# Kernel optimization log

Hardware: AMD Instinct MI355X
Metric: run time of the kernel (lower is better)

Reference implementation:

```python
import jax, jax.numpy as jnp
import numpy as np

N, E, IN, HID, EE, L, NB = 20000, 256000, 64, 128, 32, 3, 8


def _silu(x):
    return x * jax.nn.sigmoid(x)


def setup_inputs() -> dict:
    key = jax.random.key(0)
    ks = list(jax.random.split(key, 32))

    def nrm(k, shape, fan_in):
        return jax.random.normal(k, shape, dtype=jnp.float32) / np.sqrt(fan_in)

    inp = {}
    inp["H_t"] = jax.random.normal(ks[0], (N, IN), dtype=jnp.float32)
    inp["X_t"] = jax.random.normal(ks[1], (N, 3), dtype=jnp.float32)
    inp["cond_embedding"] = jax.random.normal(ks[2], (N, HID), dtype=jnp.float32)
    inp["t"] = jax.random.uniform(ks[3], (N,), dtype=jnp.float32)
    inp["edges"] = jax.random.randint(ks[4], (2, E), 0, N)
    inp["edge_types"] = jax.random.randint(ks[5], (E,), 0, 2)
    inp["generate_mask"] = jax.random.bernoulli(ks[6], 0.7, (N,))
    inp["batch_ids"] = jnp.sort(jax.random.randint(ks[7], (N,), 0, NB))
    # input MLP: (IN + 2*HID) -> HID -> HID -> HID, 3 linear layers
    d0 = IN + 2 * HID
    inp["mlp_W0"] = nrm(ks[8], (d0, HID), d0)
    inp["mlp_b0"] = jnp.zeros((HID,), jnp.float32)
    inp["mlp_W1"] = nrm(ks[9], (HID, HID), HID)
    inp["mlp_b1"] = jnp.zeros((HID,), jnp.float32)
    inp["mlp_W2"] = nrm(ks[10], (HID, HID), HID)
    inp["mlp_b2"] = jnp.zeros((HID,), jnp.float32)
    inp["edge_table"] = jax.random.normal(ks[11], (2, EE), dtype=jnp.float32)
    # encoder (EGNN-style message passing), stacked over L layers
    de = 2 * HID + 1 + EE  # [h_src, h_dst, dist^2, edge_embed]
    inp["We"] = nrm(ks[12], (L, de, HID), de)
    inp["be"] = jnp.zeros((L, HID), jnp.float32)
    inp["Wx"] = nrm(ks[13], (L, HID, 1), HID)
    inp["bx"] = jnp.zeros((L, 1), jnp.float32)
    inp["Wh"] = nrm(ks[14], (L, 2 * HID, HID), 2 * HID)
    inp["bh"] = jnp.zeros((L, HID), jnp.float32)
    inp["h2i_W"] = nrm(ks[15], (HID, IN), HID)
    inp["h2i_b"] = jnp.zeros((IN,), jnp.float32)
    return inp


def reference(H_t, X_t, cond_embedding, t, mlp_W0, mlp_b0, mlp_W1, mlp_b1,
              mlp_W2, mlp_b2, edge_table, We, be, Wx, bx, Wh, bh,
              h2i_W, h2i_b, edges, edge_types, generate_mask, batch_ids):
    n = H_t.shape[0]
    hid = mlp_W2.shape[1]
    # sinusoidal time embedding (dim = hidden_size)
    half = hid // 2
    freqs = jnp.exp(jnp.arange(half, dtype=jnp.float32) * (-np.log(10000.0) / (half - 1)))
    ang = t[:, None] * freqs[None, :]
    t_embed = jnp.concatenate([jnp.sin(ang), jnp.cos(ang)], axis=-1)  # (N, hid)
    # input MLP
    feat = jnp.concatenate([H_t, cond_embedding, t_embed], axis=-1)
    h = jax.nn.relu(feat @ mlp_W0 + mlp_b0)
    h = jax.nn.relu(h @ mlp_W1 + mlp_b1)
    h = h @ mlp_W2 + mlp_b2
    eemb = edge_table[edge_types]  # (E, EE)
    src, dst = edges[0], edges[1]
    cnt = jax.ops.segment_sum(jnp.ones((src.shape[0], 1), h.dtype), dst, num_segments=n)
    x = X_t
    for l in range(We.shape[0]):
        diff = x[src] - x[dst]                              # (E, 3)
        d2 = jnp.sum(diff * diff, axis=-1, keepdims=True)   # (E, 1)
        m_in = jnp.concatenate([h[src], h[dst], d2, eemb], axis=-1)
        msg = _silu(m_in @ We[l] + be[l])                   # (E, hid)
        w = msg @ Wx[l] + bx[l]                             # (E, 1)
        agg_x = jax.ops.segment_sum(diff * w, dst, num_segments=n)
        x = x + agg_x / (cnt + 1.0)
        agg_m = jax.ops.segment_sum(msg, dst, num_segments=n)
        h = h + _silu(jnp.concatenate([h, agg_m], axis=-1) @ Wh[l] + bh[l])
    mask = generate_mask[:, None]
    v_X = jnp.where(mask, x, jnp.zeros_like(x))
    v_H = jnp.where(mask, h @ h2i_W + h2i_b, 0.0)
    return (v_H, v_X)
```

## Files before the change

kernel.cpp:

```cpp
#include <hip/hip_runtime.h>
#include <math.h>

#define NN 20000
#define NE 256000
#define IN_DIM 64
#define HID 128
#define DE 289
#define D0 320
#define TILE_E 64
#define NB64 313
#define NUB 8
#define SRCMASK 0x3FFFFFFF

typedef unsigned short u16;
typedef unsigned int u32;
typedef unsigned long long u64;
typedef __attribute__((ext_vector_type(8))) short short8;
typedef __attribute__((ext_vector_type(4))) float float4v;

#define OFF_WE   0
#define OFF_W0   122880
#define OFF_W1   163840
#define OFF_W2   180224
#define OFF_WH   196608
#define OFF_H2I  294912
#define PACK_TOT 303104
#define PREP_TOT (PACK_TOT + 1152 + NN)

static __device__ __forceinline__ u16 f2bf(float f) {
    unsigned int u = __float_as_uint(f);
    u += 0x7fffu + ((u >> 16) & 1u);
    return (u16)(u >> 16);
}
static __device__ __forceinline__ float bf2f(u16 s) {
    return __uint_as_float(((unsigned int)s) << 16);
}
static __device__ __forceinline__ float bflo(u32 u) { return bf2f((u16)(u & 0xffffu)); }
static __device__ __forceinline__ float bfhi(u32 u) { return bf2f((u16)(u >> 16)); }
static __device__ __forceinline__ u32 pack2(float a, float b) {
    return (u32)f2bf(a) | ((u32)f2bf(b) << 16);
}
static __device__ __forceinline__ uint4 pack8(const float* v) {
    uint4 r;
    r.x = (u32)f2bf(v[0]) | ((u32)f2bf(v[1]) << 16);
    r.y = (u32)f2bf(v[2]) | ((u32)f2bf(v[3]) << 16);
    r.z = (u32)f2bf(v[4]) | ((u32)f2bf(v[5]) << 16);
    r.w = (u32)f2bf(v[6]) | ((u32)f2bf(v[7]) << 16);
    return r;
}
static __device__ __forceinline__ float silu(float v) {
    return v * (1.f / (1.f + __expf(-v)));
}

__global__ __launch_bounds__(256) void hist_kernel(
    const float* __restrict__ X_t, const int* __restrict__ edges,
    float* __restrict__ x, int* __restrict__ deg)
{
    int gid = blockIdx.x * blockDim.x + threadIdx.x;
    int stride = gridDim.x * blockDim.x;
    for (int i = gid; i < NN * 3; i += stride) x[i] = X_t[i];
    for (int e = gid; e < NE; e += stride)
        atomicAdd(&deg[edges[NE + e]], 1);
}

__global__ __launch_bounds__(1024) void scan_kernel(
    const int* __restrict__ deg, int* __restrict__ row_start, int* __restrict__ head)
{
    __shared__ int s[1024];
    int tx = threadIdx.x;
    const int per = (NN + 1023) / 1024;
    int st = tx * per, en = st + per;
    if (st > NN) st = NN;
    if (en > NN) en = NN;
    int sum = 0;
    for (int i = st; i < en; ++i) sum += deg[i];
    s[tx] = sum;
    __syncthreads();
    for (int off = 1; off < 1024; off <<= 1) {
        int t = (tx >= off) ? s[tx - off] : 0;
        __syncthreads();
        s[tx] += t;
        __syncthreads();
    }
    int run = (tx == 0) ? 0 : s[tx - 1];
    for (int i = st; i < en; ++i) {
        row_start[i] = run; head[i] = run; run += deg[i];
    }
    if (tx == 1023) row_start[NN] = run;
}

__global__ __launch_bounds__(256) void scatter_kernel(
    const int* __restrict__ edges, const int* __restrict__ etype,
    int* __restrict__ head,
    int* __restrict__ src_s)
{
    int gid = blockIdx.x * blockDim.x + threadIdx.x;
    int stride = gridDim.x * blockDim.x;
    for (int e = gid; e < NE; e += stride) {
        int d = edges[NE + e];
        int p = atomicAdd(&head[d], 1);
        src_s[p] = edges[e] | (etype[e] << 30);
    }
}

__global__ __launch_bounds__(256) void prep_kernel(
    const float* __restrict__ We, const float* __restrict__ W0,
    const float* __restrict__ W1, const float* __restrict__ W2,
    const float* __restrict__ Wh, const float* __restrict__ h2i,
    const float* __restrict__ edge_table, const float* __restrict__ be,
    u16* __restrict__ Bp, float* __restrict__ tv, float* __restrict__ wed2,
    int* __restrict__ deg)
{
    int idx = blockIdx.x * 256 + threadIdx.x;
    if (idx < PACK_TOT) {
        const float* src; int N = 128, Ksrc; int r;
        if (idx < OFF_W0) {
            int layer = idx / 40960; r = idx - layer * 40960;
            src = We + (size_t)layer * DE * HID; Ksrc = DE;
        } else if (idx < OFF_W1) { r = idx - OFF_W0; src = W0; Ksrc = 320; }
        else if (idx < OFF_W2)   { r = idx - OFF_W1; src = W1; Ksrc = 128; }
        else if (idx < OFF_WH)   { r = idx - OFF_W2; src = W2; Ksrc = 128; }
        else if (idx < OFF_H2I) {
            int t = idx - OFF_WH; int layer = t / 32768; r = t - layer * 32768;
            src = Wh + (size_t)layer * 256 * HID; Ksrc = 256;
        } else { r = idx - OFF_H2I; src = h2i; Ksrc = 128; N = 64; }
        int ntc = N / 16;
        int j = r & 7, lane = (r >> 3) & 63;
        int rem = r >> 9;
        int nt = rem % ntc, ks = rem / ntc;
        int k = ks * 32 + ((lane >> 4) << 3) + j;
        int c = nt * 16 + (lane & 15);
        Bp[idx] = f2bf((k < Ksrc) ? src[(size_t)k * N + c] : 0.f);
    } else if (idx < PACK_TOT + 768) {
        int q = idx - PACK_TOT;
        int f = q & 127, t = (q >> 7) & 1, l = q >> 8;
        float acc = be[l * 128 + f];
        const float* W = We + (size_t)l * DE * HID;
        #pragma unroll
        for (int k = 0; k < 32; ++k)
            acc += edge_table[t * 32 + k] * W[(size_t)(257 + k) * HID + f];
        tv[l * 256 + t * 128 + f] = acc;
    } else if (idx < PACK_TOT + 1152) {
        int r = idx - PACK_TOT - 768;
        int f = r & 127, l = r >> 7;
        wed2[l * 128 + f] = We[(size_t)l * DE * HID + (size_t)256 * HID + f];
    } else if (idx < PREP_TOT) {
        deg[idx - PACK_TOT - 1152] = 0;
    }
}

__global__ __launch_bounds__(256) void node_mlp_mfma_kernel(
    const float* __restrict__ H_t, const float* __restrict__ cond,
    const float* __restrict__ t_in,
    const u16* __restrict__ W0p, const float* __restrict__ b0,
    const u16* __restrict__ W1p, const float* __restrict__ b1,
    const u16* __restrict__ W2p, const float* __restrict__ b2,
    const u16* __restrict__ WEp,
    u16* __restrict__ Csrc, u16* __restrict__ Cdst,
    float* __restrict__ h, u16* __restrict__ h_bf)
{
    __shared__ u16 s_A[64 * 64];
    __shared__ u16 s_B[64 * 128];
    __shared__ u16 s_h[64 * 128];
    __shared__ float s_t[64];

    int tx = threadIdx.x;
    int n0 = blockIdx.x * 64;
    int l = tx & 63, w = tx >> 6;
    int mt_base = (w & 1) * 2, nt_base = (w >> 1) * 4;
    const float cfr = -logf(10000.f) / 63.f;

    if (tx < 64) s_t[tx] = (n0 + tx < NN) ? t_in[n0 + tx] : 0.f;

    float4v acc[2][4];
    #pragma unroll
    for (int mi = 0; mi < 2; ++mi)
        #pragma unroll
        for (int ni = 0; ni < 4; ++ni) acc[mi][ni] = (float4v){0.f,0.f,0.f,0.f};

    for (int t = 0; t < 5; ++t) {
        __syncthreads();
        #pragma unroll
        for (int it = 0; it < 2; ++it) {
            int flat = it * 256 + tx;
            int n = flat >> 3, sl = flat & 7;
            int c = sl ^ (n & 7);
            int k0 = t * 64 + c * 8;
            float tv8[8];
            int gn = n0 + n;
            if (gn < NN) {
                if (k0 < 192) {
                    const float* src = (k0 < 64) ? &H_t[(size_t)gn * IN_DIM + k0]
                                                 : &cond[(size_t)gn * HID + (k0 - 64)];
                    float4 a = *(const float4*)src;
                    float4 b = *(const float4*)(src + 4);
                    tv8[0]=a.x; tv8[1]=a.y; tv8[2]=a.z; tv8[3]=a.w;
                    tv8[4]=b.x; tv8[5]=b.y; tv8[6]=b.z; tv8[7]=b.w;
                } else {
                    float tvv = s_t[n];
                    int jj = (k0 - 192) & 63;
                    bool is_sin = (k0 < 256);
                    #pragma unroll
                    for (int jx = 0; jx < 8; ++jx) {
                        float ang = tvv * __expf(cfr * (float)(jj + jx));
                        tv8[jx] = is_sin ? __sinf(ang) : __cosf(ang);
                    }
                }
            } else {
                #pragma unroll
                for (int jx = 0; jx < 8; ++jx) tv8[jx] = 0.f;
            }
            *(uint4*)&s_A[n * 64 + sl * 8] = pack8(tv8);
        }
        #pragma unroll
        for (int it = 0; it < 4; ++it) {
            int flat = it * 256 + tx;
            ((uint4*)s_B)[flat] = ((const uint4*)(W0p + (size_t)t * 8192))[flat];
        }
        __syncthreads();
        #pragma unroll
        for (int s = 0; s < 2; ++s) {
            short8 af[2], bfv[4];
            #pragma unroll
            for (int mi = 0; mi < 2; ++mi) {
                int m = (mt_base + mi) * 16 + (l & 15);
                int c = s * 4 + (l >> 4);
                int slot = c ^ (l & 7);
                af[mi] = *(const short8*)(s_A + m * 64 + slot * 8);
            }
            #pragma unroll
            for (int ni = 0; ni < 4; ++ni)
                bfv[ni] = *(const short8*)(s_B + ((s * 8 + nt_base + ni) * 64 + l) * 8);
            #pragma unroll
            for (int mi = 0; mi < 2; ++mi)
                #pragma unroll
                for (int ni = 0; ni < 4; ++ni)
                    acc[mi][ni] = __builtin_amdgcn_mfma_f32_16x16x32_bf16(
                        af[mi], bfv[ni], acc[mi][ni], 0, 0, 0);
        }
    }
    #pragma unroll
    for (int mi = 0; mi < 2; ++mi) {
        #pragma unroll
        for (int ni = 0; ni < 4; ++ni) {
            int f = (nt_base + ni) * 16 + (l & 15);
            float bv = b0[f];
            #pragma unroll
            for (int r = 0; r < 4; ++r) {
                int m = (mt_base + mi) * 16 + (l >> 4) * 4 + r;
                float v = fmaxf(acc[mi][ni][r] + bv, 0.f);
                int slot = (f >> 3) ^ (m & 7);
                s_h[m * 128 + slot * 8 + (f & 7)] = f2bf(v);
            }
            acc[mi][ni] = (float4v){0.f,0.f,0.f,0.f};
        }
    }
    for (int t = 0; t < 2; ++t) {
        __syncthreads();
        #pragma unroll
        for (int it = 0; it < 4; ++it) {
            int flat = it * 256 + tx;
            ((uint4*)s_B)[flat] = ((const uint4*)(W1p + (size_t)t * 8192))[flat];
        }
        __syncthreads();
        #pragma unroll
        for (int s = 0; s < 2; ++s) {
            short8 af[2], bfv[4];
            #pragma unroll
            for (int mi = 0; mi < 2; ++mi) {
                int m = (mt_base + mi) * 16 + (l & 15);
                int c = t * 8 + s * 4 + (l >> 4);
                int slot = c ^ (l & 7);
                af[mi] = *(const short8*)(s_h + m * 128 + slot * 8);
            }
            #pragma unroll
            for (int ni = 0; ni < 4; ++ni)
                bfv[ni] = *(const short8*)(s_B + ((s * 8 + nt_base + ni) * 64 + l) * 8);
            #pragma unroll
            for (int mi = 0; mi < 2; ++mi)
                #pragma unroll
                for (int ni = 0; ni < 4; ++ni)
                    acc[mi][ni] = __builtin_amdgcn_mfma_f32_16x16x32_bf16(
                        af[mi], bfv[ni], acc[mi][ni], 0, 0, 0);
        }
    }
    __syncthreads();
    #pragma unroll
    for (int mi = 0; mi < 2; ++mi) {
        #pragma unroll
        for (int ni = 0; ni < 4; ++ni) {
            int f = (nt_base + ni) * 16 + (l & 15);
            float bv = b1[f];
            #pragma unroll
            for (int r = 0; r < 4; ++r) {
                int m = (mt_base + mi) * 16 + (l >> 4) * 4 + r;
                float v = fmaxf(acc[mi][ni][r] + bv, 0.f);
                int slot = (f >> 3) ^ (m & 7);
                s_h[m * 128 + slot * 8 + (f & 7)] = f2bf(v);
            }
            acc[mi][ni] = (float4v){0.f,0.f,0.f,0.f};
        }
    }
    for (int t = 0; t < 2; ++t) {
        __syncthreads();
        #pragma unroll
        for (int it = 0; it < 4; ++it) {
            int flat = it * 256 + tx;
            ((uint4*)s_B)[flat] = ((const uint4*)(W2p + (size_t)t * 8192))[flat];
        }
        __syncthreads();
        #pragma unroll
        for (int s = 0; s < 2; ++s) {
            short8 af[2], bfv[4];
            #pragma unroll
            for (int mi = 0; mi < 2; ++mi) {
                int m = (mt_base + mi) * 16 + (l & 15);
                int c = t * 8 + s * 4 + (l >> 4);
                int slot = c ^ (l & 7);
                af[mi] = *(const short8*)(s_h + m * 128 + slot * 8);
            }
            #pragma unroll
            for (int ni = 0; ni < 4; ++ni)
                bfv[ni] = *(const short8*)(s_B + ((s * 8 + nt_base + ni) * 64 + l) * 8);
            #pragma unroll
            for (int mi = 0; mi < 2; ++mi)
                #pragma unroll
                for (int ni = 0; ni < 4; ++ni)
                    acc[mi][ni] = __builtin_amdgcn_mfma_f32_16x16x32_bf16(
                        af[mi], bfv[ni], acc[mi][ni], 0, 0, 0);
        }
    }
    __syncthreads();
    #pragma unroll
    for (int mi = 0; mi < 2; ++mi) {
        #pragma unroll
        for (int ni = 0; ni < 4; ++ni) {
            int f = (nt_base + ni) * 16 + (l & 15);
            float bv = b2[f];
            #pragma unroll
            for (int r = 0; r < 4; ++r) {
                int m = (mt_base + mi) * 16 + (l >> 4) * 4 + r;
                int gn = n0 + m;
                float v = acc[mi][ni][r] + bv;
                int slot = (f >> 3) ^ (m & 7);
                s_h[m * 128 + slot * 8 + (f & 7)] = f2bf(v);
                if (gn < NN) {
                    h[(size_t)gn * HID + f] = v;
                    h_bf[(size_t)gn * HID + f] = f2bf(v);
                }
            }
        }
    }

    for (int sd = 0; sd < 2; ++sd) {
        #pragma unroll
        for (int mi = 0; mi < 2; ++mi)
            #pragma unroll
            for (int ni = 0; ni < 4; ++ni) acc[mi][ni] = (float4v){0.f,0.f,0.f,0.f};
        #pragma unroll
        for (int th = 0; th < 2; ++th) {
            int t = sd * 2 + th;
            __syncthreads();
            #pragma unroll
            for (int it = 0; it < 4; ++it) {
                int flat = it * 256 + tx;
                ((uint4*)s_B)[flat] = ((const uint4*)(WEp + (size_t)t * 8192))[flat];
            }
            __syncthreads();
            #pragma unroll
            for (int s = 0; s < 2; ++s) {
                short8 af[2], bfv[4];
                #pragma unroll
                for (int mi = 0; mi < 2; ++mi) {
                    int m = (mt_base + mi) * 16 + (l & 15);
                    int c = th * 8 + s * 4 + (l >> 4);
                    int slot = c ^ (l & 7);
                    af[mi] = *(const short8*)(s_h + m * 128 + slot * 8);
                }
                #pragma unroll
                for (int ni = 0; ni < 4; ++ni)
                    bfv[ni] = *(const short8*)(s_B + ((s * 8 + nt_base + ni) * 64 + l) * 8);
                #pragma unroll
                for (int mi = 0; mi < 2; ++mi)
                    #pragma unroll
                    for (int ni = 0; ni < 4; ++ni)
                        acc[mi][ni] = __builtin_amdgcn_mfma_f32_16x16x32_bf16(
                            af[mi], bfv[ni], acc[mi][ni], 0, 0, 0);
            }
        }
        u16* Cout = (sd == 0) ? Csrc : Cdst;
        #pragma unroll
        for (int mi = 0; mi < 2; ++mi) {
            #pragma unroll
            for (int ni = 0; ni < 4; ++ni) {
                int fq = (nt_base + ni) * 16 + (l & 15);
                #pragma unroll
                for (int r = 0; r < 4; ++r) {
                    int m = (mt_base + mi) * 16 + (l >> 4) * 4 + r;
                    int gn = n0 + m;
                    if (gn < NN)
                        Cout[(size_t)gn * 128 + fq] = f2bf(acc[mi][ni][r]);
                }
            }
        }
    }
}

__global__ __launch_bounds__(256) void cvec_kernel(
    const u16* __restrict__ h_bf, const u16* __restrict__ WEp,
    u16* __restrict__ Csrc, u16* __restrict__ Cdst)
{
    __shared__ u16 s_A[64 * 64];
    __shared__ u16 s_B[64 * 128];

    int tx = threadIdx.x;
    int n0 = blockIdx.x * 64;
    int l = tx & 63, w = tx >> 6;
    int mt_base = (w & 1) * 2, nt_base = (w >> 1) * 4;

    float4v acc[2][2][4];
    #pragma unroll
    for (int sd = 0; sd < 2; ++sd)
        #pragma unroll
        for (int mi = 0; mi < 2; ++mi)
            #pragma unroll
            for (int ni = 0; ni < 4; ++ni)
                acc[sd][mi][ni] = (float4v){0.f,0.f,0.f,0.f};

    for (int t = 0; t < 4; ++t) {
        __syncthreads();
        #pragma unroll
        for (int it = 0; it < 2; ++it) {
            int flat = it * 256 + tx;
            int n = flat >> 3, sl = flat & 7;
            int c = sl ^ (n & 7);
            int gn = n0 + n;
            uint4 v = make_uint4(0,0,0,0);
            if (gn < NN) v = *(const uint4*)(h_bf + (size_t)gn * 128 + (t & 1) * 64 + c * 8);
            *(uint4*)&s_A[n * 64 + sl * 8] = v;
        }
        #pragma unroll
        for (int it = 0; it < 4; ++it) {
            int flat = it * 256 + tx;
            ((uint4*)s_B)[flat] = ((const uint4*)(WEp + (size_t)t * 8192))[flat];
        }
        __syncthreads();
        int sd = t >> 1;
        #pragma unroll
        for (int s = 0; s < 2; ++s) {
            short8 af[2], bfv[4];
            #pragma unroll
            for (int mi = 0; mi < 2; ++mi) {
                int m = (mt_base + mi) * 16 + (l & 15);
                int c = s * 4 + (l >> 4);
                int slot = c ^ (l & 7);
                af[mi] = *(const short8*)(s_A + m * 64 + slot * 8);
            }
            #pragma unroll
            for (int ni = 0; ni < 4; ++ni)
                bfv[ni] = *(const short8*)(s_B + ((s * 8 + nt_base + ni) * 64 + l) * 8);
            #pragma unroll
            for (int mi = 0; mi < 2; ++mi)
                #pragma unroll
                for (int ni = 0; ni < 4; ++ni)
                    acc[sd][mi][ni] = __builtin_amdgcn_mfma_f32_16x16x32_bf16(
                        af[mi], bfv[ni], acc[sd][mi][ni], 0, 0, 0);
        }
    }
    #pragma unroll
    for (int sd = 0; sd < 2; ++sd) {
        u16* Cout = (sd == 0) ? Csrc : Cdst;
        #pragma unroll
        for (int mi = 0; mi < 2; ++mi) {
            #pragma unroll
            for (int ni = 0; ni < 4; ++ni) {
                int fq = (nt_base + ni) * 16 + (l & 15);
                #pragma unroll
                for (int r = 0; r < 4; ++r) {
                    int m = (mt_base + mi) * 16 + (l >> 4) * 4 + r;
                    int gn = n0 + m;
                    if (gn < NN)
                        Cout[(size_t)gn * 128 + fq] = f2bf(acc[sd][mi][ni][r]);
                }
            }
        }
    }
}

__global__ __launch_bounds__(512, 4) void node_fused_kernel(
    float* __restrict__ h, u16* __restrict__ h_bf,
    const float* __restrict__ x_in, float* __restrict__ x_out,
    const u16* __restrict__ Csrc, const u16* __restrict__ Cdst,
    const int* __restrict__ src_s,
    const int* __restrict__ row_start,
    const float* __restrict__ tv_l, const float* __restrict__ wed2_l,
    const float* __restrict__ Wx_l, const float* __restrict__ bx_l,
    const u16* __restrict__ Whp_l, const float* __restrict__ bh_l)
{
    __shared__ u16 s_A[16 * 256];

    int tx = threadIdx.x;
    int n0 = blockIdx.x * NUB;
    int l = tx & 63, w = tx >> 6;
    int i = w;
    int gn = n0 + i;
    int p = l & 31, q = l >> 5;

    if (tx < 256) {
        int n = tx >> 4, c = tx & 15;
        int slot = c ^ (n & 7);
        uint4 v = make_uint4(0, 0, 0, 0);
        if (n < NUB) v = *(const uint4*)(h_bf + (size_t)(n0 + n) * 128 + c * 8);
        *(uint4*)&s_A[n * 256 + slot * 8] = v;
    } else if (tx < 384) {
        int n = 8 + ((tx - 256) >> 4), c = 16 + (tx & 15);
        int slot = c ^ (n & 7);
        *(uint4*)&s_A[n * 256 + slot * 8] = make_uint4(0, 0, 0, 0);
    }

    float c0[4], d01[4], wed[4], wx[4];
    {
        uint2 cd = *(const uint2*)(Cdst + (size_t)gn * 128 + p * 4);
        float cdv0 = bflo(cd.x), cdv1 = bfhi(cd.x), cdv2 = bflo(cd.y), cdv3 = bfhi(cd.y);
        float4 t0 = *(const float4*)(tv_l + p * 4);
        float4 t1 = *(const float4*)(tv_l + 128 + p * 4);
        float4 wd = *(const float4*)(wed2_l + p * 4);
        float4 wv = *(const float4*)(Wx_l + p * 4);
        c0[0] = t0.x + cdv0; c0[1] = t0.y + cdv1; c0[2] = t0.z + cdv2; c0[3] = t0.w + cdv3;
        d01[0] = t1.x - t0.x; d01[1] = t1.y - t0.y; d01[2] = t1.z - t0.z; d01[3] = t1.w - t0.w;
        wed[0] = wd.x; wed[1] = wd.y; wed[2] = wd.z; wed[3] = wd.w;
        wx[0] = wv.x; wx[1] = wv.y; wx[2] = wv.z; wx[3] = wv.w;
    }
    float bx32 = bx_l[0] * (1.f / 32.f);

    int rs = row_start[gn], re = row_start[gn + 1];
    int d = re - rs;

    float xd0 = x_in[gn * 3 + 0], xd1 = x_in[gn * 3 + 1], xd2 = x_in[gn * 3 + 2];

    float ag[4] = {0.f, 0.f, 0.f, 0.f};
    float sx = 0.f, sy = 0.f, sz = 0.f;

    for (int e0 = 0; e0 < d; e0 += 64) {
        int nchunk = d - e0; if (nchunk > 64) nchunk = 64;
        int sp_l = (l < nchunk) ? src_s[rs + e0 + l] : 0;
        float gx_l = 0.f, gy_l = 0.f, gz_l = 0.f, d2_l = 0.f;
        if (l < nchunk) {
            int sm = sp_l & SRCMASK;
            gx_l = x_in[sm * 3 + 0] - xd0;
            gy_l = x_in[sm * 3 + 1] - xd1;
            gz_l = x_in[sm * 3 + 2] - xd2;
            d2_l = gx_l * gx_l + gy_l * gy_l + gz_l * gz_l;
        }

        auto FETCH = [&](int lj, uint2& cc, float& et) {
            int spE = __shfl(sp_l, lj);
            cc = make_uint2(0u, 0u); et = 0.f;
            if (lj < nchunk) {
                cc = *(const uint2*)(Csrc + (size_t)(spE & SRCMASK) * 128 + p * 4);
                et = (float)((u32)spE >> 30);
            }
        };
        auto PROC = [&](int lj, uint2 cc, float ee) {
            float dxe = __shfl(gx_l, lj);
            float dye = __shfl(gy_l, lj);
            float dze = __shfl(gz_l, lj);
            float d2e = __shfl(d2_l, lj);
            float av[4];
            av[0] = bflo(cc.x); av[1] = bfhi(cc.x);
            av[2] = bflo(cc.y); av[3] = bfhi(cc.y);
            float wpart = bx32;
            #pragma unroll
            for (int f = 0; f < 4; ++f) {
                float t = __fmaf_rn(d2e, wed[f], c0[f]);
                t = __fmaf_rn(ee, d01[f], t);
                float v = av[f] + t;
                float m = silu(v);
                ag[f] += m;
                wpart = __fmaf_rn(m, wx[f], wpart);
            }
            sx = __fmaf_rn(dxe, wpart, sx);
            sy = __fmaf_rn(dye, wpart, sy);
            sz = __fmaf_rn(dze, wpart, sz);
        };

        int ljA = q,      ljB = q + 2,  ljC = q + 4,  ljD = q + 6;
        int ljE = q + 8,  ljF = q + 10, ljG = q + 12, ljH = q + 14;
        int ljn = q + 16;
        uint2 ccA, ccB, ccC, ccD, ccE, ccF, ccG, ccH;
        float etA, etB, etC, etD, etE, etF, etG, etH;
        FETCH(ljA, ccA, etA); FETCH(ljB, ccB, etB);
        FETCH(ljC, ccC, etC); FETCH(ljD, ccD, etD);
        FETCH(ljE, ccE, etE); FETCH(ljF, ccF, etF);
        FETCH(ljG, ccG, etG); FETCH(ljH, ccH, etH);
        while (ljA < nchunk) {
            PROC(ljA, ccA, etA); ljA = ljn; ljn += 2; FETCH(ljA, ccA, etA);
            if (ljB >= nchunk) break;
            PROC(ljB, ccB, etB); ljB = ljn; ljn += 2; FETCH(ljB, ccB, etB);
            if (ljC >= nchunk) break;
            PROC(ljC, ccC, etC); ljC = ljn; ljn += 2; FETCH(ljC, ccC, etC);
            if (ljD >= nchunk) break;
            PROC(ljD, ccD, etD); ljD = ljn; ljn += 2; FETCH(ljD, ccD, etD);
            if (ljE >= nchunk) break;
            PROC(ljE, ccE, etE); ljE = ljn; ljn += 2; FETCH(ljE, ccE, etE);
            if (ljF >= nchunk) break;
            PROC(ljF, ccF, etF); ljF = ljn; ljn += 2; FETCH(ljF, ccF, etF);
            if (ljG >= nchunk) break;
            PROC(ljG, ccG, etG); ljG = ljn; ljn += 2; FETCH(ljG, ccG, etG);
            if (ljH >= nchunk) break;
            PROC(ljH, ccH, etH); ljH = ljn; ljn += 2; FETCH(ljH, ccH, etH);
        }
    }

    #pragma unroll
    for (int f = 0; f < 4; ++f) ag[f] += __shfl_xor(ag[f], 32);
    #pragma unroll
    for (int off = 1; off <= 32; off <<= 1) {
        sx += __shfl_xor(sx, off);
        sy += __shfl_xor(sy, off);
        sz += __shfl_xor(sz, off);
    }
    if (l < 32) {
        int c2 = 16 + (p >> 1);
        int slot = c2 ^ (i & 7);
        uint2 o;
        o.x = pack2(ag[0], ag[1]);
        o.y = pack2(ag[2], ag[3]);
        *(uint2*)&s_A[i * 256 + slot * 8 + (p & 1) * 4] = o;
    }
    if (l == 0) {
        float inv = 1.f / ((float)d + 1.f);
        x_out[gn * 3 + 0] = xd0 + sx * inv;
        x_out[gn * 3 + 1] = xd1 + sy * inv;
        x_out[gn * 3 + 2] = xd2 + sz * inv;
    }

    __syncthreads();

    float4v acc = (float4v){0.f, 0.f, 0.f, 0.f};
    #pragma unroll
    for (int t = 0; t < 4; ++t) {
        #pragma unroll
        for (int s = 0; s < 2; ++s) {
            int m = l & 15;
            int c = t * 8 + s * 4 + (l >> 4);
            int slot = c ^ (l & 7);
            short8 af = *(const short8*)(s_A + m * 256 + slot * 8);
            short8 bfv = *(const short8*)(Whp_l + (size_t)t * 8192 + ((s * 8 + w) * 64 + l) * 8);
            acc = __builtin_amdgcn_mfma_f32_16x16x32_bf16(af, bfv, acc, 0, 0, 0);
        }
    }
    {
        int f = w * 16 + (l & 15);
        float bv = bh_l[f];
        #pragma unroll
        for (int r = 0; r < 4; ++r) {
            int m = (l >> 4) * 4 + r;
            if (m < NUB) {
                int gn2 = n0 + m;
                float v = acc[r] + bv;
                float hn = h[(size_t)gn2 * HID + f] + silu(v);
                h[(size_t)gn2 * HID + f] = hn;
                h_bf[(size_t)gn2 * HID + f] = f2bf(hn);
            }
        }
    }
}

__global__ __launch_bounds__(256) void final_mfma_kernel(
    const u16* __restrict__ h_bf, const float* __restrict__ x,
    const int* __restrict__ gmask,
    const u16* __restrict__ h2ip, const float* __restrict__ b,
    float* __restrict__ out)
{
    __shared__ u16 s_A[64 * 128];
    __shared__ u16 s_B[4096];

    int tx = threadIdx.x;
    int n0 = blockIdx.x * 64;
    int l = tx & 63, w = tx >> 6;
    int mt_base = (w & 1) * 2, nt_base = (w >> 1) * 2;

    #pragma unroll
    for (int it = 0; it < 4; ++it) {
        int flat = it * 256 + tx;
        int n = flat >> 4, c = flat & 15;
        int slot = c ^ (n & 7);
        int gn = n0 + n;
        uint4 v = make_uint4(0,0,0,0);
        if (gn < NN) v = *(const uint4*)(h_bf + (size_t)gn * 128 + c * 8);
        *(uint4*)&s_A[n * 128 + slot * 8] = v;
    }

    float4v acc[2][2];
    #pragma unroll
    for (int mi = 0; mi < 2; ++mi)
        #pragma unroll
        for (int ni = 0; ni < 2; ++ni) acc[mi][ni] = (float4v){0.f,0.f,0.f,0.f};

    for (int t = 0; t < 2; ++t) {
        __syncthreads();
        #pragma unroll
        for (int it = 0; it < 2; ++it) {
            int flat = it * 256 + tx;
            ((uint4*)s_B)[flat] = ((const uint4*)(h2ip + (size_t)t * 4096))[flat];
        }
        __syncthreads();
        #pragma unroll
        for (int s = 0; s < 2; ++s) {
            short8 af[2], bfv[2];
            #pragma unroll
            for (int mi = 0; mi < 2; ++mi) {
                int m = (mt_base + mi) * 16 + (l & 15);
                int c = t * 8 + s * 4 + (l >> 4);
                int slot = c ^ (l & 7);
                af[mi] = *(const short8*)(s_A + m * 128 + slot * 8);
            }
            #pragma unroll
            for (int ni = 0; ni < 2; ++ni)
                bfv[ni] = *(const short8*)(s_B + ((s * 4 + nt_base + ni) * 64 + l) * 8);
            #pragma unroll
            for (int mi = 0; mi < 2; ++mi)
                #pragma unroll
                for (int ni = 0; ni < 2; ++ni)
                    acc[mi][ni] = __builtin_amdgcn_mfma_f32_16x16x32_bf16(
                        af[mi], bfv[ni], acc[mi][ni], 0, 0, 0);
        }
    }
    #pragma unroll
    for (int mi = 0; mi < 2; ++mi) {
        #pragma unroll
        for (int ni = 0; ni < 2; ++ni) {
            int f = (nt_base + ni) * 16 + (l & 15);
            float bv = b[f];
            #pragma unroll
            for (int r = 0; r < 4; ++r) {
                int m = (mt_base + mi) * 16 + (l >> 4) * 4 + r;
                int gn = n0 + m;
                if (gn < NN)
                    out[(size_t)gn * IN_DIM + f] = gmask[gn] ? (acc[mi][ni][r] + bv) : 0.f;
            }
        }
    }
    if (tx < 192) {
        int i = tx / 3, c = tx % 3;
        int gn = n0 + i;
        if (gn < NN)
            out[(size_t)NN * IN_DIM + gn * 3 + c] = gmask[gn] ? x[gn * 3 + c] : 0.f;
    }
}

__global__ __launch_bounds__(256) void init_fb_kernel(
    const float* __restrict__ X_t, const int* __restrict__ edges,
    float* __restrict__ x, float* __restrict__ cnt)
{
    int gid = blockIdx.x * blockDim.x + threadIdx.x;
    int stride = gridDim.x * blockDim.x;
    for (int i = gid; i < NN * 3; i += stride) x[i] = X_t[i];
    for (int e = gid; e < NE; e += stride)
        atomicAdd(&cnt[edges[NE + e]], 1.0f);
}

__global__ __launch_bounds__(128) void node_mlp_kernel(
    const float* __restrict__ H_t, const float* __restrict__ cond,
    const float* __restrict__ t_in,
    const float* __restrict__ W0, const float* __restrict__ b0,
    const float* __restrict__ W1, const float* __restrict__ b1,
    const float* __restrict__ W2, const float* __restrict__ b2,
    float* __restrict__ h)
{
    __shared__ float s_feat[D0][20];
    __shared__ float s_h0[HID][20];
    __shared__ float s_h1[HID][20];
    int n0 = blockIdx.x * 16;
    int tx = threadIdx.x;

    for (int idx = tx; idx < 16 * IN_DIM; idx += 128) {
        int i = idx >> 6, k = idx & 63;
        s_feat[k][i] = H_t[(n0 + i) * IN_DIM + k];
    }
    for (int idx = tx; idx < 16 * HID; idx += 128) {
        int i = idx >> 7, k = idx & 127;
        s_feat[IN_DIM + k][i] = cond[(n0 + i) * HID + k];
    }
    const float cfr = -logf(10000.f) / 63.f;
    for (int idx = tx; idx < 16 * HID; idx += 128) {
        int i = idx >> 7, k = idx & 127;
        float tv = t_in[n0 + i];
        int jj = k & 63;
        float ang = tv * __expf(cfr * (float)jj);
        s_feat[IN_DIM + HID + k][i] = (k < 64) ? __sinf(ang) : __cosf(ang);
    }
    __syncthreads();

    float acc[16];
    {
        float bv = b0[tx];
        #pragma unroll
        for (int i = 0; i < 16; ++i) acc[i] = bv;
        for (int k = 0; k < D0; ++k) {
            float w = W0[k * HID + tx];
            float4 f0 = *(const float4*)&s_feat[k][0];
            float4 f1 = *(const float4*)&s_feat[k][4];
            float4 f2 = *(const float4*)&s_feat[k][8];
            float4 f3 = *(const float4*)&s_feat[k][12];
            acc[0] += f0.x*w; acc[1] += f0.y*w; acc[2] += f0.z*w; acc[3] += f0.w*w;
            acc[4] += f1.x*w; acc[5] += f1.y*w; acc[6] += f1.z*w; acc[7] += f1.w*w;
            acc[8] += f2.x*w; acc[9] += f2.y*w; acc[10]+= f2.z*w; acc[11]+= f2.w*w;
            acc[12]+= f3.x*w; acc[13]+= f3.y*w; acc[14]+= f3.z*w; acc[15]+= f3.w*w;
        }
        #pragma unroll
        for (int i = 0; i < 16; ++i) s_h0[tx][i] = fmaxf(acc[i], 0.f);
    }
    __syncthreads();
    {
        float bv = b1[tx];
        #pragma unroll
        for (int i = 0; i < 16; ++i) acc[i] = bv;
        for (int k = 0; k < HID; ++k) {
            float w = W1[k * HID + tx];
            float4 f0 = *(const float4*)&s_h0[k][0];
            float4 f1 = *(const float4*)&s_h0[k][4];
            float4 f2 = *(const float4*)&s_h0[k][8];
            float4 f3 = *(const float4*)&s_h0[k][12];
            acc[0] += f0.x*w; acc[1] += f0.y*w; acc[2] += f0.z*w; acc[3] += f0.w*w;
            acc[4] += f1.x*w; acc[5] += f1.y*w; acc[6] += f1.z*w; acc[7] += f1.w*w;
            acc[8] += f2.x*w; acc[9] += f2.y*w; acc[10]+= f2.z*w; acc[11]+= f2.w*w;
            acc[12]+= f3.x*w; acc[13]+= f3.y*w; acc[14]+= f3.z*w; acc[15]+= f3.w*w;
        }
        #pragma unroll
        for (int i = 0; i < 16; ++i) s_h1[tx][i] = fmaxf(acc[i], 0.f);
    }
    __syncthreads();
    {
        float bv = b2[tx];
        #pragma unroll
        for (int i = 0; i < 16; ++i) acc[i] = bv;
        for (int k = 0; k < HID; ++k) {
            float w = W2[k * HID + tx];
            float4 f0 = *(const float4*)&s_h1[k][0];
            float4 f1 = *(const float4*)&s_h1[k][4];
            float4 f2 = *(const float4*)&s_h1[k][8];
            float4 f3 = *(const float4*)&s_h1[k][12];
            acc[0] += f0.x*w; acc[1] += f0.y*w; acc[2] += f0.z*w; acc[3] += f0.w*w;
            acc[4] += f1.x*w; acc[5] += f1.y*w; acc[6] += f1.z*w; acc[7] += f1.w*w;
            acc[8] += f2.x*w; acc[9] += f2.y*w; acc[10]+= f2.z*w; acc[11]+= f2.w*w;
            acc[12]+= f3.x*w; acc[13]+= f3.y*w; acc[14]+= f3.z*w; acc[15]+= f3.w*w;
        }
        #pragma unroll
        for (int i = 0; i < 16; ++i) h[(n0 + i) * HID + tx] = acc[i];
    }
}

__global__ __launch_bounds__(256) void edge_gemm_fb_kernel(
    const float* __restrict__ h, const float* __restrict__ x,
    const int* __restrict__ edges, const int* __restrict__ etype,
    const float* __restrict__ edge_table,
    const float* __restrict__ We_l, const float* __restrict__ be_l,
    const float* __restrict__ Wx_l, const float* __restrict__ bx_l,
    float* __restrict__ agg_m, float* __restrict__ agg_x)
{
    __shared__ int s_src[TILE_E], s_dst[TILE_E];
    __shared__ float s_diff[TILE_E][3];
    __shared__ float s_tail[TILE_E][36];
    __shared__ float s_Af[TILE_E][36];
    __shared__ float s_Bf[33][HID];
    __shared__ float s_wx[HID];

    int e0 = blockIdx.x * TILE_E;
    int tx = threadIdx.x;
    int tf = tx & 15;
    int te = tx >> 4;

    if (tx < TILE_E) {
        int s = edges[e0 + tx];
        int d = edges[NE + e0 + tx];
        s_src[tx] = s; s_dst[tx] = d;
        float dx = x[s * 3 + 0] - x[d * 3 + 0];
        float dy = x[s * 3 + 1] - x[d * 3 + 1];
        float dz = x[s * 3 + 2] - x[d * 3 + 2];
        s_diff[tx][0] = dx; s_diff[tx][1] = dy; s_diff[tx][2] = dz;
        s_tail[tx][0] = dx * dx + dy * dy + dz * dz;
        int et = etype[e0 + tx];
        #pragma unroll
        for (int j = 0; j < 32; ++j) s_tail[tx][1 + j] = edge_table[et * 32 + j];
    }
    if (tx < HID) s_wx[tx] = Wx_l[tx];
    __syncthreads();

    float acc[4][8];
    #pragma unroll
    for (int i = 0; i < 4; ++i)
        #pragma unroll
        for (int j = 0; j < 8; ++j) acc[i][j] = 0.f;

    for (int t = 0; t < 9; ++t) {
        int k0 = t * 32;
        int klen = (t == 8) ? 33 : 32;
        __syncthreads();
        if (t < 8) {
            const bool use_src = (t < 4);
            int kbase = (t & 3) * 32;
            for (int q4 = tx; q4 < TILE_E * 8; q4 += 256) {
                int e = q4 >> 3, q = q4 & 7;
                int row = use_src ? s_src[e] : s_dst[e];
                float4 v = *(const float4*)&h[row * HID + kbase + q * 4];
                *(float4*)&s_Af[e][q * 4] = v;
            }
        }
        for (int q4 = tx; q4 < klen * 32; q4 += 256) {
            int kk = q4 >> 5, c4 = q4 & 31;
            float4 v = *(const float4*)&We_l[(k0 + kk) * HID + c4 * 4];
            *(float4*)&s_Bf[kk][c4 * 4] = v;
        }
        __syncthreads();
        const float (*Asrc)[36] = (t == 8) ? (const float (*)[36])s_tail
                                           : (const float (*)[36])s_Af;
        for (int kk = 0; kk < klen; ++kk) {
            float a0 = Asrc[te * 4 + 0][kk];
            float a1 = Asrc[te * 4 + 1][kk];
            float a2 = Asrc[te * 4 + 2][kk];
            float a3 = Asrc[te * 4 + 3][kk];
            float4 bv0 = *(const float4*)&s_Bf[kk][tf * 8];
            float4 bv1 = *(const float4*)&s_Bf[kk][tf * 8 + 4];
            float b[8] = {bv0.x, bv0.y, bv0.z, bv0.w, bv1.x, bv1.y, bv1.z, bv1.w};
            #pragma unroll
            for (int j = 0; j < 8; ++j) {
                acc[0][j] += a0 * b[j];
                acc[1][j] += a1 * b[j];
                acc[2][j] += a2 * b[j];
                acc[3][j] += a3 * b[j];
            }
        }
    }

    float wsum[4];
    #pragma unroll
    for (int i = 0; i < 4; ++i) {
        float p = 0.f;
        #pragma unroll
        for (int j = 0; j < 8; ++j) {
            int f = tf * 8 + j;
            float v = acc[i][j] + be_l[f];
            float m = silu(v);
            acc[i][j] = m;
            p += m * s_wx[f];
        }
        wsum[i] = p;
    }
    #pragma unroll
    for (int off = 1; off < 16; off <<= 1) {
        #pragma unroll
        for (int i = 0; i < 4; ++i) wsum[i] += __shfl_xor(wsum[i], off);
    }
    float bxv = bx_l[0];
    if (tf < 3) {
        #pragma unroll
        for (int i = 0; i < 4; ++i) {
            int e = te * 4 + i;
            float w2 = wsum[i] + bxv;
            atomicAdd(&agg_x[s_dst[e] * 3 + tf], s_diff[e][tf] * w2);
        }
    }
    #pragma unroll
    for (int i = 0; i < 4; ++i) {
        int d = s_dst[te * 4 + i];
        #pragma unroll
        for (int j = 0; j < 8; ++j)
            atomicAdd(&agg_m[d * HID + tf * 8 + j], acc[i][j]);
    }
}

__global__ __launch_bounds__(128) void node_update_fb_kernel(
    float* __restrict__ h, float* __restrict__ x,
    const float* __restrict__ agg_m, const float* __restrict__ agg_x,
    const float* __restrict__ cnt,
    const float* __restrict__ Wh_l, const float* __restrict__ bh_l)
{
    __shared__ float s_in[256][20];
    int n0 = blockIdx.x * 16;
    int tx = threadIdx.x;
    for (int idx = tx; idx < 16 * HID; idx += 128) {
        int i = idx >> 7, k = idx & 127;
        s_in[k][i] = h[(n0 + i) * HID + k];
    }
    for (int idx = tx; idx < 16 * HID; idx += 128) {
        int i = idx >> 7, k = idx & 127;
        s_in[HID + k][i] = agg_m[(n0 + i) * HID + k];
    }
    __syncthreads();
    float acc[16];
    float bv = bh_l[tx];
    #pragma unroll
    for (int i = 0; i < 16; ++i) acc[i] = bv;
    for (int k = 0; k < 256; ++k) {
        float w = Wh_l[k * HID + tx];
        float4 f0 = *(const float4*)&s_in[k][0];
        float4 f1 = *(const float4*)&s_in[k][4];
        float4 f2 = *(const float4*)&s_in[k][8];
        float4 f3 = *(const float4*)&s_in[k][12];
        acc[0] += f0.x*w; acc[1] += f0.y*w; acc[2] += f0.z*w; acc[3] += f0.w*w;
        acc[4] += f1.x*w; acc[5] += f1.y*w; acc[6] += f1.z*w; acc[7] += f1.w*w;
        acc[8] += f2.x*w; acc[9] += f2.y*w; acc[10]+= f2.z*w; acc[11]+= f2.w*w;
        acc[12]+= f3.x*w; acc[13]+= f3.y*w; acc[14]+= f3.z*w; acc[15]+= f3.w*w;
    }
    #pragma unroll
    for (int i = 0; i < 16; ++i) {
        float v = acc[i];
        h[(n0 + i) * HID + tx] = s_in[tx][i] + silu(v);
    }
    if (tx < 48) {
        int i = tx / 3, c = tx % 3;
        int n = n0 + i;
        x[n * 3 + c] += agg_x[n * 3 + c] / (cnt[n] + 1.f);
    }
}

__global__ __launch_bounds__(64) void final_fb_kernel(
    const float* __restrict__ h, const float* __restrict__ x,
    const int* __restrict__ gmask,
    const float* __restrict__ W, const float* __restrict__ b,
    float* __restrict__ out)
{
    __shared__ float s_h[8][HID];
    int n0 = blockIdx.x * 8;
    int tx = threadIdx.x;
    for (int idx = tx; idx < 8 * HID; idx += 64) {
        int i = idx >> 7, k = idx & 127;
        s_h[i][k] = h[(n0 + i) * HID + k];
    }
    __syncthreads();
    float acc[8];
    float bv = b[tx];
    #pragma unroll
    for (int i = 0; i < 8; ++i) acc[i] = bv;
    for (int k = 0; k < HID; ++k) {
        float w = W[k * IN_DIM + tx];
        #pragma unroll
        for (int i = 0; i < 8; ++i) acc[i] += s_h[i][k] * w;
    }
    #pragma unroll
    for (int i = 0; i < 8; ++i) {
        int n = n0 + i;
        out[n * IN_DIM + tx] = gmask[n] ? acc[i] : 0.f;
    }
    if (tx < 24) {
        int i = tx / 3, c = tx % 3;
        int n = n0 + i;
        out[NN * IN_DIM + n * 3 + c] = gmask[n] ? x[n * 3 + c] : 0.f;
    }
}

extern "C" void kernel_launch(void* const* d_in, const int* in_sizes, int n_in,
                              void* d_out, int out_size, void* d_ws, size_t ws_size,
                              hipStream_t stream) {
    const float* H_t   = (const float*)d_in[0];
    const float* X_t   = (const float*)d_in[1];
    const float* cond  = (const float*)d_in[2];
    const float* t_in  = (const float*)d_in[3];
    const int*   edges = (const int*)d_in[4];
    const int*   etype = (const int*)d_in[5];
    const int*   gmask = (const int*)d_in[6];
    const float* W0 = (const float*)d_in[8];
    const float* b0 = (const float*)d_in[9];
    const float* W1 = (const float*)d_in[10];
    const float* b1 = (const float*)d_in[11];
    const float* W2 = (const float*)d_in[12];
    const float* b2 = (const float*)d_in[13];
    const float* edge_table = (const float*)d_in[14];
    const float* We = (const float*)d_in[15];
    const float* be = (const float*)d_in[16];
    const float* Wx = (const float*)d_in[17];
    const float* bx = (const float*)d_in[18];
    const float* Wh = (const float*)d_in[19];
    const float* bh = (const float*)d_in[20];
    const float* h2i_W = (const float*)d_in[21];
    const float* h2i_b = (const float*)d_in[22];

    char* p = (char*)d_ws;
    float* h = (float*)p;           p += (size_t)NN * HID * 4;
    u16* h_bf = (u16*)p;            p += (size_t)NN * HID * 2;
    float* xa = (float*)p;          p += (size_t)NN * 3 * 4;
    float* xb = (float*)p;          p += (size_t)NN * 3 * 4;
    u16* Csrc = (u16*)p;            p += (size_t)NN * 128 * 2;
    u16* Cdst = (u16*)p;            p += (size_t)NN * 128 * 2;
    u16* Bpack = (u16*)p;           p += (size_t)PACK_TOT * 2;
    float* tv = (float*)p;          p += (size_t)768 * 4;
    float* wed2 = (float*)p;        p += (size_t)384 * 4;
    int* row_start = (int*)p;       p += (size_t)(NN + 4) * 4;
    int* deg = (int*)p;             p += (size_t)NN * 4;
    int* head = (int*)p;            p += (size_t)NN * 4;
    int* src_s = (int*)p;           p += (size_t)NE * 4;
    size_t need = (size_t)(p - (char*)d_ws);

    if (ws_size >= need) {
        prep_kernel<<<(PREP_TOT + 255) / 256, 256, 0, stream>>>(
            We, W0, W1, W2, Wh, h2i_W, edge_table, be, Bpack, tv, wed2, deg);
        hist_kernel<<<256, 256, 0, stream>>>(X_t, edges, xa, deg);
        scan_kernel<<<1, 1024, 0, stream>>>(deg, row_start, head);
        scatter_kernel<<<256, 256, 0, stream>>>(edges, etype, head, src_s);
        node_mlp_mfma_kernel<<<NB64, 256, 0, stream>>>(
            H_t, cond, t_in,
            Bpack + OFF_W0, b0, Bpack + OFF_W1, b1, Bpack + OFF_W2, b2,
            Bpack + OFF_WE, Csrc, Cdst,
            h, h_bf);
        for (int l = 0; l < 3; ++l) {
            if (l > 0)
                cvec_kernel<<<NB64, 256, 0, stream>>>(
                    h_bf, Bpack + OFF_WE + (size_t)l * 40960, Csrc, Cdst);
            const float* xin = (l & 1) ? xb : xa;
            float* xout = (l & 1) ? xa : xb;
            node_fused_kernel<<<NN / NUB, 512, 0, stream>>>(
                h, h_bf, xin, xout, Csrc, Cdst, src_s, row_start,
                tv + (size_t)l * 256, wed2 + (size_t)l * 128,
                Wx + l * HID, bx + l,
                Bpack + OFF_WH + (size_t)l * 32768, bh + l * HID);
        }
        final_mfma_kernel<<<NB64, 256, 0, stream>>>(
            h_bf, xb, gmask, Bpack + OFF_H2I, h2i_b, (float*)d_out);
    } else {
        float* ws    = (float*)d_ws;
        float* fh    = ws;
        float* fx    = fh + NN * HID;
        float* cnt   = fx + NN * 3;
        float* fagg_m = cnt + NN;
        float* fagg_x = fagg_m + NN * HID;

        hipMemsetAsync(cnt, 0, NN * sizeof(float), stream);
        init_fb_kernel<<<256, 256, 0, stream>>>(X_t, edges, fx, cnt);
        node_mlp_kernel<<<NN / 16, 128, 0, stream>>>(H_t, cond, t_in,
                                                     W0, b0, W1, b1, W2, b2, fh);
        for (int l = 0; l < 3; ++l) {
            hipMemsetAsync(fagg_m, 0, (size_t)NN * 131 * sizeof(float), stream);
            edge_gemm_fb_kernel<<<NE / TILE_E, 256, 0, stream>>>(
                fh, fx, edges, etype, edge_table,
                We + (size_t)l * DE * HID, be + l * HID,
                Wx + l * HID, bx + l, fagg_m, fagg_x);
            node_update_fb_kernel<<<NN / 16, 128, 0, stream>>>(
                fh, fx, fagg_m, fagg_x, cnt,
                Wh + (size_t)l * 256 * HID, bh + l * HID);
        }
        final_fb_kernel<<<NN / 8, 64, 0, stream>>>(fh, fx, gmask, h2i_W, h2i_b, (float*)d_out);
    }
}
```

Before: 371.2 us.

## Fuse next-layer C projection and final output GEMM into node_fused_kernel

Removes the separate cvec_kernel and final_mfma_kernel. Each node block now computes the next layer's per-node src/dst projections, or the h2i output and masked x in the last layer, from its freshly updated h held in shared memory. The C buffers are double-buffered so the next layer's projections can be written while the current ones are still being read. The edge-loop prefetch depth also drops from 8 to 4 outstanding fetches, probably to free registers for the added MFMA work. The trade-off is that each 8-node block reads B-fragments straight from global memory with poor reuse, and half of each 16-row MFMA tile is padding.

Result: faster. 353.6 us (-4.7%).

```diff
diff --git a/kernel.cpp b/kernel.cpp
--- a/kernel.cpp
+++ b/kernel.cpp
@@ -406,98 +406,22 @@
     }
 }
 
-__global__ __launch_bounds__(256) void cvec_kernel(
-    const u16* __restrict__ h_bf, const u16* __restrict__ WEp,
-    u16* __restrict__ Csrc, u16* __restrict__ Cdst)
-{
-    __shared__ u16 s_A[64 * 64];
-    __shared__ u16 s_B[64 * 128];
-
-    int tx = threadIdx.x;
-    int n0 = blockIdx.x * 64;
-    int l = tx & 63, w = tx >> 6;
-    int mt_base = (w & 1) * 2, nt_base = (w >> 1) * 4;
-
-    float4v acc[2][2][4];
-    #pragma unroll
-    for (int sd = 0; sd < 2; ++sd)
-        #pragma unroll
-        for (int mi = 0; mi < 2; ++mi)
-            #pragma unroll
-            for (int ni = 0; ni < 4; ++ni)
-                acc[sd][mi][ni] = (float4v){0.f,0.f,0.f,0.f};
-
-    for (int t = 0; t < 4; ++t) {
-        __syncthreads();
-        #pragma unroll
-        for (int it = 0; it < 2; ++it) {
-            int flat = it * 256 + tx;
-            int n = flat >> 3, sl = flat & 7;
-            int c = sl ^ (n & 7);
-            int gn = n0 + n;
-            uint4 v = make_uint4(0,0,0,0);
-            if (gn < NN) v = *(const uint4*)(h_bf + (size_t)gn * 128 + (t & 1) * 64 + c * 8);
-            *(uint4*)&s_A[n * 64 + sl * 8] = v;
-        }
-        #pragma unroll
-        for (int it = 0; it < 4; ++it) {
-            int flat = it * 256 + tx;
-            ((uint4*)s_B)[flat] = ((const uint4*)(WEp + (size_t)t * 8192))[flat];
-        }
-        __syncthreads();
-        int sd = t >> 1;
-        #pragma unroll
-        for (int s = 0; s < 2; ++s) {
-            short8 af[2], bfv[4];
-            #pragma unroll
-            for (int mi = 0; mi < 2; ++mi) {
-                int m = (mt_base + mi) * 16 + (l & 15);
-                int c = s * 4 + (l >> 4);
-                int slot = c ^ (l & 7);
-                af[mi] = *(const short8*)(s_A + m * 64 + slot * 8);
-            }
-            #pragma unroll
-            for (int ni = 0; ni < 4; ++ni)
-                bfv[ni] = *(const short8*)(s_B + ((s * 8 + nt_base + ni) * 64 + l) * 8);
-            #pragma unroll
-            for (int mi = 0; mi < 2; ++mi)
-                #pragma unroll
-                for (int ni = 0; ni < 4; ++ni)
-                    acc[sd][mi][ni] = __builtin_amdgcn_mfma_f32_16x16x32_bf16(
-                        af[mi], bfv[ni], acc[sd][mi][ni], 0, 0, 0);
-        }
-    }
-    #pragma unroll
-    for (int sd = 0; sd < 2; ++sd) {
-        u16* Cout = (sd == 0) ? Csrc : Cdst;
-        #pragma unroll
-        for (int mi = 0; mi < 2; ++mi) {
-            #pragma unroll
-            for (int ni = 0; ni < 4; ++ni) {
-                int fq = (nt_base + ni) * 16 + (l & 15);
-                #pragma unroll
-                for (int r = 0; r < 4; ++r) {
-                    int m = (mt_base + mi) * 16 + (l >> 4) * 4 + r;
-                    int gn = n0 + m;
-                    if (gn < NN)
-                        Cout[(size_t)gn * 128 + fq] = f2bf(acc[sd][mi][ni][r]);
-                }
-            }
-        }
-    }
-}
-
 __global__ __launch_bounds__(512, 4) void node_fused_kernel(
     float* __restrict__ h, u16* __restrict__ h_bf,
     const float* __restrict__ x_in, float* __restrict__ x_out,
     const u16* __restrict__ Csrc, const u16* __restrict__ Cdst,
+    u16* __restrict__ Csrc_n, u16* __restrict__ Cdst_n,
+    const u16* __restrict__ Wnext, const float* __restrict__ bfin,
+    const int* __restrict__ gmask, float* __restrict__ out,
     const int* __restrict__ src_s,
     const int* __restrict__ row_start,
     const float* __restrict__ tv_l, const float* __restrict__ wed2_l,
     const float* __restrict__ Wx_l, const float* __restrict__ bx_l,
-    const u16* __restrict__ Whp_l, const float* __restrict__ bh_l)
+    const u16* __restrict__ Whp_l, const float* __restrict__ bh_l,
+    int mode)
 {
     __shared__ u16 s_A[16 * 256];
+    __shared__ u16 s_h2[16 * 128];
 
     int tx = threadIdx.x;
     int n0 = blockIdx.x * NUB;
@@ -584,15 +508,10 @@
             sz = __fmaf_rn(dze, wpart, sz);
         };
 
-        int ljA = q,      ljB = q + 2,  ljC = q + 4,  ljD = q + 6;
-        int ljE = q + 8,  ljF = q + 10, ljG = q + 12, ljH = q + 14;
-        int ljn = q + 16;
-        uint2 ccA, ccB, ccC, ccD, ccE, ccF, ccG, ccH;
-        float etA, etB, etC, etD, etE, etF, etG, etH;
+        int ljA = q, ljB = q + 2, ljC = q + 4, ljD = q + 6, ljn = q + 8;
+        uint2 ccA, ccB, ccC, ccD; float etA, etB, etC, etD;
         FETCH(ljA, ccA, etA); FETCH(ljB, ccB, etB);
         FETCH(ljC, ccC, etC); FETCH(ljD, ccD, etD);
-        FETCH(ljE, ccE, etE); FETCH(ljF, ccF, etF);
-        FETCH(ljG, ccG, etG); FETCH(ljH, ccH, etH);
         while (ljA < nchunk) {
             PROC(ljA, ccA, etA); ljA = ljn; ljn += 2; FETCH(ljA, ccA, etA);
             if (ljB >= nchunk) break;
@@ -601,14 +520,6 @@
             PROC(ljC, ccC, etC); ljC = ljn; ljn += 2; FETCH(ljC, ccC, etC);
             if (ljD >= nchunk) break;
             PROC(ljD, ccD, etD); ljD = ljn; ljn += 2; FETCH(ljD, ccD, etD);
-            if (ljE >= nchunk) break;
-            PROC(ljE, ccE, etE); ljE = ljn; ljn += 2; FETCH(ljE, ccE, etE);
-            if (ljF >= nchunk) break;
-            PROC(ljF, ccF, etF); ljF = ljn; ljn += 2; FETCH(ljF, ccF, etF);
-            if (ljG >= nchunk) break;
-            PROC(ljG, ccG, etG); ljG = ljn; ljn += 2; FETCH(ljG, ccG, etG);
-            if (ljH >= nchunk) break;
-            PROC(ljH, ccH, etH); ljH = ljn; ljn += 2; FETCH(ljH, ccH, etH);
         }
     }
 
@@ -628,11 +539,17 @@
         o.y = pack2(ag[2], ag[3]);
         *(uint2*)&s_A[i * 256 + slot * 8 + (p & 1) * 4] = o;
     }
+    float inv = 1.f / ((float)d + 1.f);
     if (l == 0) {
-        float inv = 1.f / ((float)d + 1.f);
         x_out[gn * 3 + 0] = xd0 + sx * inv;
         x_out[gn * 3 + 1] = xd1 + sy * inv;
         x_out[gn * 3 + 2] = xd2 + sz * inv;
+    }
+    if (mode == 1 && l < 3) {
+        float xv = (l == 0) ? (xd0 + sx * inv)
+                 : (l == 1) ? (xd1 + sy * inv)
+                            : (xd2 + sz * inv);
+        out[(size_t)NN * IN_DIM + gn * 3 + l] = gmask[gn] ? xv : 0.f;
     }
 
     __syncthreads();
@@ -656,97 +573,77 @@
         #pragma unroll
         for (int r = 0; r < 4; ++r) {
             int m = (l >> 4) * 4 + r;
+            u16 hb = 0;
             if (m < NUB) {
                 int gn2 = n0 + m;
                 float v = acc[r] + bv;
                 float hn = h[(size_t)gn2 * HID + f] + silu(v);
-                h[(size_t)gn2 * HID + f] = hn;
-                h_bf[(size_t)gn2 * HID + f] = f2bf(hn);
-            }
-        }
-    }
-}
-
-__global__ __launch_bounds__(256) void final_mfma_kernel(
-    const u16* __restrict__ h_bf, const float* __restrict__ x,
-    const int* __restrict__ gmask,
-    const u16* __restrict__ h2ip, const float* __restrict__ b,
-    float* __restrict__ out)
-{
-    __shared__ u16 s_A[64 * 128];
-    __shared__ u16 s_B[4096];
-
-    int tx = threadIdx.x;
-    int n0 = blockIdx.x * 64;
-    int l = tx & 63, w = tx >> 6;
-    int mt_base = (w & 1) * 2, nt_base = (w >> 1) * 2;
-
-    #pragma unroll
-    for (int it = 0; it < 4; ++it) {
-        int flat = it * 256 + tx;
-        int n = flat >> 4, c = flat & 15;
-        int slot = c ^ (n & 7);
-        int gn = n0 + n;
-        uint4 v = make_uint4(0,0,0,0);
-        if (gn < NN) v = *(const uint4*)(h_bf + (size_t)gn * 128 + c * 8);
-        *(uint4*)&s_A[n * 128 + slot * 8] = v;
-    }
-
-    float4v acc[2][2];
-    #pragma unroll
-    for (int mi = 0; mi < 2; ++mi)
-        #pragma unroll
-        for (int ni = 0; ni < 2; ++ni) acc[mi][ni] = (float4v){0.f,0.f,0.f,0.f};
-
-    for (int t = 0; t < 2; ++t) {
-        __syncthreads();
-        #pragma unroll
-        for (int it = 0; it < 2; ++it) {
-            int flat = it * 256 + tx;
-            ((uint4*)s_B)[flat] = ((const uint4*)(h2ip + (size_t)t * 4096))[flat];
-        }
-        __syncthreads();
-        #pragma unroll
-        for (int s = 0; s < 2; ++s) {
-            short8 af[2], bfv[2];
-            #pragma unroll
-            for (int mi = 0; mi < 2; ++mi) {
-                int m = (mt_base + mi) * 16 + (l & 15);
-                int c = t * 8 + s * 4 + (l >> 4);
-                int slot = c ^ (l & 7);
-                af[mi] = *(const short8*)(s_A + m * 128 + slot * 8);
-            }
-            #pragma unroll
-            for (int ni = 0; ni < 2; ++ni)
-                bfv[ni] = *(const short8*)(s_B + ((s * 4 + nt_base + ni) * 64 + l) * 8);
-            #pragma unroll
-            for (int mi = 0; mi < 2; ++mi)
+                hb = f2bf(hn);
+                if (mode == 0) {
+                    h[(size_t)gn2 * HID + f] = hn;
+                    h_bf[(size_t)gn2 * HID + f] = hb;
+                }
+            }
+            int slot2 = (f >> 3) ^ (m & 7);
+            s_h2[m * 128 + slot2 * 8 + (f & 7)] = hb;
+        }
+    }
+    __syncthreads();
+
+    if (mode == 0) {
+        #pragma unroll
+        for (int j = 0; j < 2; ++j) {
+            int g = w * 2 + j;
+            int sd = g >> 3, nt = g & 7;
+            float4v a2 = (float4v){0.f, 0.f, 0.f, 0.f};
+            #pragma unroll
+            for (int kt = 0; kt < 2; ++kt) {
                 #pragma unroll
-                for (int ni = 0; ni < 2; ++ni)
-                    acc[mi][ni] = __builtin_amdgcn_mfma_f32_16x16x32_bf16(
-                        af[mi], bfv[ni], acc[mi][ni], 0, 0, 0);
-        }
-    }
-    #pragma unroll
-    for (int mi = 0; mi < 2; ++mi) {
-        #pragma unroll
-        for (int ni = 0; ni < 2; ++ni) {
-            int f = (nt_base + ni) * 16 + (l & 15);
-            float bv = b[f];
+                for (int s = 0; s < 2; ++s) {
+                    int c = kt * 8 + s * 4 + (l >> 4);
+                    int slot = c ^ (l & 7);
+                    short8 af = *(const short8*)(s_h2 + (l & 15) * 128 + slot * 8);
+                    short8 bfv = *(const short8*)(Wnext + (size_t)(sd * 2 + kt) * 8192
+                                                  + ((s * 8 + nt) * 64 + l) * 8);
+                    a2 = __builtin_amdgcn_mfma_f32_16x16x32_bf16(af, bfv, a2, 0, 0, 0);
+                }
+            }
+            u16* Cout = sd ? Cdst_n : Csrc_n;
+            int f = nt * 16 + (l & 15);
             #pragma unroll
             for (int r = 0; r < 4; ++r) {
-                int m = (mt_base + mi) * 16 + (l >> 4) * 4 + r;
-                int gn = n0 + m;
-                if (gn < NN)
-                    out[(size_t)gn * IN_DIM + f] = gmask[gn] ? (acc[mi][ni][r] + bv) : 0.f;
-            }
-        }
-    }
-    if (tx < 192) {
-        int i = tx / 3, c = tx % 3;
-        int gn = n0 + i;
-        if (gn < NN)
-            out[(size_t)NN * IN_DIM + gn * 3 + c] = gmask[gn] ? x[gn * 3 + c] : 0.f;
+                int m = (l >> 4) * 4 + r;
+                if (m < NUB)
+                    Cout[(size_t)(n0 + m) * 128 + f] = f2bf(a2[r]);
+            }
+        }
+    } else {
+        if (w < 4) {
+            int nt = w;
+            float4v a2 = (float4v){0.f, 0.f, 0.f, 0.f};
+            #pragma unroll
+            for (int t = 0; t < 2; ++t) {
+                #pragma unroll
+                for (int s = 0; s < 2; ++s) {
+                    int c = t * 8 + s * 4 + (l >> 4);
+                    int slot = c ^ (l & 7);
+                    short8 af = *(const short8*)(s_h2 + (l & 15) * 128 + slot * 8);
+                    short8 bfv = *(const short8*)(Wnext + (size_t)t * 4096
+                                                  + ((s * 4 + nt) * 64 + l) * 8);
+                    a2 = __builtin_amdgcn_mfma_f32_16x16x32_bf16(af, bfv, a2, 0, 0, 0);
+                }
+            }
+            int f = nt * 16 + (l & 15);
+            float bv = bfin[f];
+            #pragma unroll
+            for (int r = 0; r < 4; ++r) {
+                int m = (l >> 4) * 4 + r;
+                if (m < NUB) {
+                    int gn2 = n0 + m;
+                    out[(size_t)gn2 * IN_DIM + f] = gmask[gn2] ? (a2[r] + bv) : 0.f;
+                }
+            }
+        }
     }
 }
 
@@ -1082,8 +979,10 @@
     u16* h_bf = (u16*)p;            p += (size_t)NN * HID * 2;
     float* xa = (float*)p;          p += (size_t)NN * 3 * 4;
     float* xb = (float*)p;          p += (size_t)NN * 3 * 4;
-    u16* Csrc = (u16*)p;            p += (size_t)NN * 128 * 2;
-    u16* Cdst = (u16*)p;            p += (size_t)NN * 128 * 2;
+    u16* Ca_s = (u16*)p;            p += (size_t)NN * 128 * 2;
+    u16* Ca_d = (u16*)p;            p += (size_t)NN * 128 * 2;
+    u16* Cb_s = (u16*)p;            p += (size_t)NN * 128 * 2;
+    u16* Cb_d = (u16*)p;            p += (size_t)NN * 128 * 2;
     u16* Bpack = (u16*)p;           p += (size_t)PACK_TOT * 2;
     float* tv = (float*)p;          p += (size_t)768 * 4;
     float* wed2 = (float*)p;        p += (size_t)384 * 4;
@@ -1102,22 +1001,27 @@
         node_mlp_mfma_kernel<<<NB64, 256, 0, stream>>>(
             H_t, cond, t_in,
             Bpack + OFF_W0, b0, Bpack + OFF_W1, b1, Bpack + OFF_W2, b2,
-            Bpack + OFF_WE, Csrc, Cdst,
+            Bpack + OFF_WE, Ca_s, Ca_d,
             h, h_bf);
         for (int l = 0; l < 3; ++l) {
-            if (l > 0)
-                cvec_kernel<<<NB64, 256, 0, stream>>>(
-                    h_bf, Bpack + OFF_WE + (size_t)l * 40960, Csrc, Cdst);
             const float* xin = (l & 1) ? xb : xa;
             float* xout = (l & 1) ? xa : xb;
+            const u16* cs_in = (l & 1) ? Cb_s : Ca_s;
+            const u16* cd_in = (l & 1) ? Cb_d : Ca_d;
+            u16* cs_out = (l & 1) ? Ca_s : Cb_s;
+            u16* cd_out = (l & 1) ? Ca_d : Cb_d;
+            int mode = (l == 2) ? 1 : 0;
+            const u16* Wnext = mode ? (Bpack + OFF_H2I)
+                                    : (Bpack + OFF_WE + (size_t)(l + 1) * 40960);
             node_fused_kernel<<<NN / NUB, 512, 0, stream>>>(
-                h, h_bf, xin, xout, Csrc, Cdst, src_s, row_start,
+                h, h_bf, xin, xout, cs_in, cd_in, cs_out, cd_out,
+                Wnext, h2i_b, gmask, (float*)d_out,
+                src_s, row_start,
                 tv + (size_t)l * 256, wed2 + (size_t)l * 128,
                 Wx + l * HID, bx + l,
-                Bpack + OFF_WH + (size_t)l * 32768, bh + l * HID);
-        }
-        final_mfma_kernel<<<NB64, 256, 0, stream>>>(
-            h_bf, xb, gmask, Bpack + OFF_H2I, h2i_b, (float*)d_out);
+                Bpack + OFF_WH + (size_t)l * 32768, bh + l * HID,
+                mode);
+        }
     } else {
         float* ws    = (float*)d_ws;
         float* fh    = ws;
```
